# Optimization experiments

Hardware: AMD Instinct MI355X
Metric: run time of the kernel (lower is better)

Reference implementation:

```python
import jax, jax.numpy as jnp
import numpy as np

ROPE_THETA = 10000.0

def _rope(t):
    # t: (B, S, H, D) -- rotate-half RoPE over last dim
    B, S, H, D = t.shape
    inv_freq = 1.0 / (ROPE_THETA ** (jnp.arange(0, D, 2, dtype=jnp.float32) / D))  # (D/2,)
    ang = jnp.arange(S, dtype=jnp.float32)[:, None] * inv_freq[None, :]            # (S, D/2)
    cos = jnp.concatenate([jnp.cos(ang), jnp.cos(ang)], axis=-1)[None, :, None, :] # (1,S,1,D)
    sin = jnp.concatenate([jnp.sin(ang), jnp.sin(ang)], axis=-1)[None, :, None, :]
    t1, t2 = jnp.split(t, 2, axis=-1)
    rot = jnp.concatenate([-t2, t1], axis=-1)
    return t * cos.astype(t.dtype) + rot * sin.astype(t.dtype)

def setup_inputs() -> dict:
    key = jax.random.key(0)
    kx, kq, kk, kv, ko = jax.random.split(key, 5)
    B, S, DIM = 2, 2048, 2048
    x = jax.random.normal(kx, (B, S, DIM), dtype=jnp.float32)
    mask = jnp.tril(jnp.ones((S, S), dtype=bool))[None, None, :, :]  # causal (1,1,S,S)
    scale = DIM ** -0.5
    wq = jax.random.normal(kq, (DIM, DIM), dtype=jnp.float32) * scale
    wk = jax.random.normal(kk, (DIM, DIM), dtype=jnp.float32) * scale
    wv = jax.random.normal(kv, (DIM, DIM), dtype=jnp.float32) * scale
    wo = jax.random.normal(ko, (DIM, DIM), dtype=jnp.float32) * scale
    return {"x": x, "mask": mask, "wq": wq, "wk": wk, "wv": wv, "wo": wo}

def reference(x, mask, wq, wk, wv, wo):
    B, S, DIM = x.shape
    H = 16
    D = DIM // H
    scale = D ** -0.5
    # nn.Linear: y = x @ W.T
    q = (x @ wq.T).reshape(B, S, H, D)
    k = (x @ wk.T).reshape(B, S, H, D)
    v = (x @ wv.T).reshape(B, S, H, D)
    q = _rope(q)
    k = _rope(k)
    scores = jnp.einsum('bqhd,bkhd->bhqk', q, k) * scale
    scores = jnp.where(mask, scores, -jnp.inf)
    attn = jax.nn.softmax(scores, axis=-1)
    out = jnp.einsum('bhqk,bkhd->bqhd', attn, v).reshape(B, S, DIM)
    return out @ wo.T
```

## Files before the change

### kernel.cpp

```cpp
#include <hip/hip_runtime.h>
#include <cstdint>

typedef unsigned short u16;
typedef uint32_t u32;
typedef __attribute__((ext_vector_type(8))) short bf16x8;
typedef __attribute__((ext_vector_type(4))) float f32x4;
typedef __attribute__((ext_vector_type(16))) float f32x16;

#define DIM_ 2048
#define S_   2048
#define B_   2
#define H_   16
#define HD_  128
#define M_   (B_ * S_)

__device__ __forceinline__ u16 f2b(float f) {
  union { float f; uint32_t u; } v; v.f = f;
  uint32_t u = v.u;
  return (u16)((u + 0x7FFFu + ((u >> 16) & 1u)) >> 16);
}
__device__ __forceinline__ float b2f(u16 h) {
  union { uint32_t u; float f; } v; v.u = ((uint32_t)h) << 16;
  return v.f;
}

__device__ __forceinline__ u32 cvtpk(float lo, float hi) {
  u32 r;
  asm("v_cvt_pk_bf16_f32 %0, %1, %2" : "=v"(r) : "v"(lo), "v"(hi));
  return r;
}

typedef __attribute__((address_space(3))) u16 lds_u16_t;
typedef __attribute__((address_space(1))) const u16 glob_u16_t;

__device__ __forceinline__ void gload16(const u16* g, u16* l) {
  __builtin_amdgcn_global_load_lds((glob_u16_t*)g, (lds_u16_t*)l, 16, 0, 0);
}
#define GLD0(SRC, DST) \
  __builtin_amdgcn_global_load_lds((glob_u16_t*)(SRC), (lds_u16_t*)(DST), 16, 0, 0)

__global__ void convert5_kernel(const float* __restrict__ x, const float* __restrict__ wq,
                                const float* __restrict__ wk, const float* __restrict__ wv,
                                const float* __restrict__ wo, u16* __restrict__ xb,
                                u16* __restrict__ wqb, u16* __restrict__ wkb,
                                u16* __restrict__ wvb, u16* __restrict__ wob) {
  const float* src;
  u16* dst;
  int n;
  switch (blockIdx.y) {
    case 0: src = x;  dst = xb;  n = M_ * DIM_;   break;
    case 1: src = wq; dst = wqb; n = DIM_ * DIM_; break;
    case 2: src = wk; dst = wkb; n = DIM_ * DIM_; break;
    case 3: src = wv; dst = wvb; n = DIM_ * DIM_; break;
    default: src = wo; dst = wob; n = DIM_ * DIM_; break;
  }
  int i = (blockIdx.x * blockDim.x + threadIdx.x) * 4;
  const int stride = gridDim.x * blockDim.x * 4;
  for (; i < n; i += stride) {
    float4 v = *reinterpret_cast<const float4*>(src + i);
    uint64_t p = (uint64_t)f2b(v.x) | ((uint64_t)f2b(v.y) << 16) |
                 ((uint64_t)f2b(v.z) << 32) | ((uint64_t)f2b(v.w) << 48);
    *reinterpret_cast<uint64_t*>(dst + i) = p;
  }
}

__global__ void rope_table_kernel(float* __restrict__ cosT, float* __restrict__ sinT) {
  int i = blockIdx.x * blockDim.x + threadIdx.x;
  if (i >= 64 * S_) return;
  int d = i >> 11;
  int s = i & (S_ - 1);
  float inv = powf(10000.0f, -(float)d * (1.0f / 64.0f));
  float ang = (float)s * inv;
  cosT[i] = cosf(ang);
  sinT[i] = sinf(ang);
}

#define NT_ 32

#define LDA(DST, BASE)                                                         \
  _Pragma("unroll") for (int mi = 0; mi < 8; ++mi)                             \
      DST[mi] = *(const bf16x8*)((BASE) + mi * 1024);
#define LDB(DST, BASE)                                                         \
  _Pragma("unroll") for (int ni = 0; ni < NF_; ++ni)                           \
      DST[ni] = *(const bf16x8*)((BASE) +                                      \
          (BPERM_ ? (((ni) & 1) * 1024 + ((ni) >> 1) * 4096) : (ni) * 1024));

#define MFMA_KS(AV, BV)                                                        \
  _Pragma("unroll") for (int mi = 0; mi < 8; ++mi)                             \
    _Pragma("unroll") for (int ni = 0; ni < NF_; ++ni)                         \
        acc[mi][ni] = __builtin_amdgcn_mfma_f32_16x16x32_bf16(                 \
            AV[mi], BV[ni], acc[mi][ni], 0, 0, 0);

#define STAGE(BUF, OFFU) do {                                                  \
    _Pragma("unroll") for (int s = 0; s < ASW_; ++s)                           \
      GLD0(sA + goff + (OFFU) + s * (64 * DIM_),                               \
           lds + (BUF) * BUFSZ_ + s * 4096 + w * 512);                         \
    _Pragma("unroll") for (int s = 0; s < BSW_; ++s)                           \
      GLD0(sB + goff + (OFFU) + s * (64 * DIM_),                               \
           lds + (BUF) * BUFSZ_ + 16384 + s * 4096 + w * 512);                 \
  } while (0)

#define VMC_N() do {                                                           \
    if (ASW_ + BSW_ == 8) asm volatile("s_waitcnt vmcnt(8)" ::: "memory");     \
    else                  asm volatile("s_waitcnt vmcnt(6)" ::: "memory");     \
  } while (0)

#define TILE_N(BUF, NBUF, OFFU) do {                                           \
    LDA(a1, pAk1[BUF]); LDB(b1, pBk1[BUF]);                            \
    __builtin_amdgcn_sched_barrier(0);                                         \
    __builtin_amdgcn_s_setprio(1);                                             \
    MFMA_KS(a0, b0);                                                  \
    __builtin_amdgcn_s_setprio(0);                                             \
    asm volatile("s_waitcnt lgkmcnt(0)" ::: "memory");                         \
    __builtin_amdgcn_sched_barrier(0);                                         \
    __builtin_amdgcn_s_barrier();                                      \
    STAGE(BUF, OFFU);                                                          \
    __builtin_amdgcn_sched_barrier(0);                                         \
    VMC_N();                                                                   \
    __builtin_amdgcn_sched_barrier(0);                                         \
    __builtin_amdgcn_s_barrier();                                      \
    LDA(a0, pAk0[NBUF]); LDB(b0, pBk0[NBUF]);                          \
    __builtin_amdgcn_sched_barrier(0);                                         \
    __builtin_amdgcn_s_setprio(1);                                             \
    MFMA_KS(a1, b1);                                                  \
    __builtin_amdgcn_s_setprio(0);                                             \
  } while (0)

#define TILE_P(BUF, NBUF) do {                                   \
    LDA(a1, pAk1[BUF]); LDB(b1, pBk1[BUF]);                                    \
    __builtin_amdgcn_sched_barrier(0);                                         \
    __builtin_amdgcn_s_setprio(1);                                             \
    MFMA_KS(a0, b0);                                                           \
    __builtin_amdgcn_s_setprio(0);                                             \
    asm volatile("s_waitcnt lgkmcnt(0)" ::: "memory");                         \
    __builtin_amdgcn_sched_barrier(0);                                         \
    asm volatile("s_waitcnt vmcnt(0)" ::: "memory");                           \
    __builtin_amdgcn_sched_barrier(0);                                         \
    __builtin_amdgcn_s_barrier();                                              \
    LDA(a0, pAk0[NBUF]); LDB(b0, pBk0[NBUF]);                                  \
    __builtin_amdgcn_sched_barrier(0);                                         \
    __builtin_amdgcn_s_setprio(1);                                             \
    MFMA_KS(a1, b1);                                                           \
    __builtin_amdgcn_s_setprio(0);                                             \
  } while (0)

#define TILE_L(BUF) do {                                         \
    LDA(a1, pAk1[BUF]); LDB(b1, pBk1[BUF]);                                    \
    __builtin_amdgcn_sched_barrier(0);                                         \
    MFMA_KS(a0, b0);                                                           \
    MFMA_KS(a1, b1);                                                           \
  } while (0)

#define GEMM_V2_BODY(BN_, BPERM__)                                             \
  constexpr int NF_ = (BN_) / 64;                                              \
  constexpr int BPERM_ = (BPERM__);                                            \
  constexpr int ASW_ = 4;                                                      \
  constexpr int BSW_ = (BN_) / 64;                                             \
  constexpr int BUFSZ_ = 16384 + (BN_) * 64;                                   \
  const int tid = threadIdx.x;                                                 \
  const int lane = tid & 63;                                                   \
  const int w = tid >> 6;                                                      \
  const int wm = w >> 2, wn = w & 3;                                           \
  const int l15 = lane & 15, lg = lane >> 4;                                   \
  const int goff = (w * 8 + (lane >> 3)) * DIM_ + ((lane & 7) ^ (lane >> 3)) * 8; \
  const int x7 = l15 & 7;                                                      \
  const int lr0 = l15 * 64 + ((lg ^ x7) * 8);                                  \
  const int lr1 = l15 * 64 + (((4 | lg) ^ x7) * 8);                            \
  const int bbase = BPERM_ ? ((wn >> 1) * 8192 + (wn & 1) * 2048)              \
                           : (wn * ((BN_) * 16));                              \
  const u16* pAk0[2] = {lds + wm * 8192 + lr0, lds + BUFSZ_ + wm * 8192 + lr0};\
  const u16* pAk1[2] = {lds + wm * 8192 + lr1, lds + BUFSZ_ + wm * 8192 + lr1};\
  const u16* pBk0[2] = {lds + 16384 + bbase + lr0,                             \
                        lds + BUFSZ_ + 16384 + bbase + lr0};                   \
  const u16* pBk1[2] = {lds + 16384 + bbase + lr1,                             \
                        lds + BUFSZ_ + 16384 + bbase + lr1};                   \
  f32x4 acc[8][NF_];                                                           \
  _Pragma("unroll") for (int i = 0; i < 8; ++i)                                \
    _Pragma("unroll") for (int j = 0; j < NF_; ++j)                            \
        acc[i][j] = (f32x4){0.f, 0.f, 0.f, 0.f};                               \
  bf16x8 a0[8], a1[8], b0[NF_], b1[NF_];                                       \
  STAGE(0, 0);                                                                 \
  STAGE(1, 64);                                                                \
  __builtin_amdgcn_sched_barrier(0);                                           \
  VMC_N();                                                                     \
  __builtin_amdgcn_sched_barrier(0);                                           \
  __builtin_amdgcn_s_barrier();                                                \
  LDA(a0, pAk0[0]); LDB(b0, pBk0[0]);                                          \
  for (int t = 0; t < NT_ - 2; t += 2) {                                       \
    TILE_N(0, 1, 128);                                                         \
    TILE_N(1, 0, 192);                                                         \
    sA += 128; sB += 128;                                                      \
  }                                                                            \
  TILE_P(0, 1);                                                                \
  TILE_L(1);

__global__ __launch_bounds__(512, 2) void gemm256_qkv_kernel(
    const u16* __restrict__ xb, const u16* __restrict__ wqb, const u16* __restrict__ wkb,
    const u16* __restrict__ wvb, u16* __restrict__ qb, u16* __restrict__ kb,
    u16* __restrict__ vb, const float* __restrict__ cosT, const float* __restrict__ sinT) {
  __shared__ __align__(16) u16 lds[65536];

  const int bid = blockIdx.x;
  const int logical = (bid & 7) * 48 + (bid >> 3);
  const int mt = logical / 24;
  const int rem = logical % 24;
  const int z = rem >> 3;
  const int nt = rem & 7;
  const u16* Wm = (z == 0) ? wqb : (z == 1) ? wkb : wvb;
  u16* out = (z == 0) ? qb : (z == 1) ? kb : vb;

  const u16* sA = xb + (size_t)(mt * 256) * DIM_;
  const u16* sB = Wm + (size_t)(nt * 256) * DIM_;

  GEMM_V2_BODY(256, 1)

  const int colbase = nt * 256 + (wn >> 1) * 128 + (wn & 1) * 32;
  if (z < 2) {
#pragma unroll
    for (int mi = 0; mi < 8; ++mi) {
      const int row = mt * 256 + wm * 128 + mi * 16 + lg * 4;
      const int s = row & (S_ - 1);
#pragma unroll
      for (int ni = 0; ni < 2; ++ni) {
        const int d = (wn & 1) * 32 + ni * 16 + l15;
        const float4 c4 = *(const float4*)(cosT + d * S_ + s);
        const float4 s4 = *(const float4*)(sinT + d * S_ + s);
        const float cc[4]  = {c4.x, c4.y, c4.z, c4.w};
        const float ssn[4] = {s4.x, s4.y, s4.z, s4.w};
        u16* p = out + (size_t)row * DIM_ + colbase + ni * 16 + l15;
#pragma unroll
        for (int r = 0; r < 4; ++r) {
          const float t1 = acc[mi][ni][r];
          const float t2 = acc[mi][ni + 2][r];
          p[(size_t)r * DIM_]      = f2b(t1 * cc[r] - t2 * ssn[r]);
          p[(size_t)r * DIM_ + 64] = f2b(t2 * cc[r] + t1 * ssn[r]);
        }
      }
    }
  } else {
#pragma unroll
    for (int mi = 0; mi < 8; ++mi)
#pragma unroll
      for (int ni = 0; ni < 4; ++ni) {
        const int row = mt * 256 + wm * 128 + mi * 16 + lg * 4;
        const int col = colbase + (ni & 1) * 16 + (ni >> 1) * 64 + l15;
#pragma unroll
        for (int r = 0; r < 4; ++r)
          out[(size_t)(row + r) * DIM_ + col] = f2b(acc[mi][ni][r]);
      }
  }
}

__global__ __launch_bounds__(512, 2) void gemm_out_v2_kernel(const u16* __restrict__ A,
                                                             const u16* __restrict__ W,
                                                             float* __restrict__ Cf) {
  __shared__ __align__(16) u16 lds[49152];
  const int bid = blockIdx.x;
  const int logical = (bid & 7) * 32 + (bid >> 3);
  const int mt = logical >> 4;
  const int nt = logical & 15;

  const u16* sA = A + (size_t)(mt * 256) * DIM_;
  const u16* sB = W + (size_t)(nt * 128) * DIM_;

  GEMM_V2_BODY(128, 0)

#pragma unroll
  for (int mi = 0; mi < 8; ++mi)
#pragma unroll
    for (int ni = 0; ni < 2; ++ni) {
      const int row = mt * 256 + wm * 128 + mi * 16 + lg * 4;
      const int col = nt * 128 + wn * 32 + ni * 16 + l15;
#pragma unroll
      for (int r = 0; r < 4; ++r)
        Cf[(size_t)(row + r) * DIM_ + col] = acc[mi][ni][r];
    }
}

#define CEXP 0.12751744f

__global__ __launch_bounds__(256, 2) void attn_kernel(const u16* __restrict__ q,
                                                      const u16* __restrict__ k,
                                                      const u16* __restrict__ v,
                                                      u16* __restrict__ ao) {
  __shared__ __align__(16) u16 smem[32768];
  u16* kTl = smem;
  u16* vTl = smem + 16384;

  const int qt   = blockIdx.z ? (int)blockIdx.x : (int)(gridDim.x - 1 - blockIdx.x);
  const int head = blockIdx.y;
  const int b    = blockIdx.z;
  const int t = threadIdx.x;
  const int lane = t & 63;
  const int w = t >> 6;
  const int l31 = lane & 31;
  const int hi = lane >> 5;
  const int kxor = (lane & 7) << 3;
  const int qrow0 = qt * 128 + w * 32;
  const size_t bS = (size_t)b * S_;

  bf16x8 qf[8];
  {
    const u16* qrow = q + (bS + qrow0 + l31) * DIM_ + head * HD_;
#pragma unroll
    for (int st = 0; st < 8; ++st)
      qf[st] = *(const bf16x8*)(qrow + st * 16 + hi * 8);
  }

  f32x16 accO[4];
#pragma unroll
  for (int db = 0; db < 4; ++db)
#pragma unroll
    for (int rr = 0; rr < 16; ++rr) accO[db][rr] = 0.f;
  float m = -1e30f, l = 0.f;

  const int tmax_w = 2 * qt + (w >> 1);
  const int ttend = 2 * qt + 1;

  bf16x8 vv[4];

  auto stageK = [&](int buf, int tt) {
#pragma unroll
    for (int p = 0; p < 4; ++p) {
      const int cid = p * 256 + w * 64 + lane;
      const int kr = cid >> 4;
      const int cg = (cid & 15) ^ (kr & 7);
      gload16(k + (bS + tt * 64 + kr) * DIM_ + head * HD_ + cg * 8,
              kTl + buf * 8192 + (p * 256 + w * 64) * 8);
    }
  };
  auto loadV = [&](int tt) {
#pragma unroll
    for (int p = 0; p < 4; ++p) {
      const int dchunk = p * 4 + w;
      vv[p] = *(const bf16x8*)(v + (bS + tt * 64 + lane) * DIM_ + head * HD_ + dchunk * 8);
    }
  };
  auto writeV = [&](int buf) {
#pragma unroll
    for (int p = 0; p < 4; ++p) {
      const int dchunk = p * 4 + w;
#pragma unroll
      for (int j = 0; j < 8; ++j) {
        const int d = dchunk * 8 + j;
        vTl[buf * 8192 + d * 64 + (lane ^ ((d & 7) << 3))] = (u16)vv[p][j];
      }
    }
  };

  stageK(0, 0);
  loadV(0);
  writeV(0);
  __syncthreads();

  for (int tt = 0; tt <= ttend; ++tt) {
    const int cur = tt & 1;
    const int alt = cur ^ 1;

    if (tt + 1 <= ttend) {
      stageK(alt, tt + 1);
      loadV(tt + 1);
    }

    if (tt <= tmax_w) {
      const u16* kB = kTl + cur * 8192;
      const u16* vB = vTl + cur * 8192;
      f32x16 sA, sB;
#pragma unroll
      for (int rr = 0; rr < 16; ++rr) { sA[rr] = 0.f; sB[rr] = 0.f; }
      __builtin_amdgcn_s_setprio(1);
#pragma unroll
      for (int st = 0; st < 8; ++st) {
        const int dc = st * 16 + hi * 8;
        bf16x8 k0 = *(const bf16x8*)(kB + l31 * 128 + (dc ^ kxor));
        bf16x8 k1 = *(const bf16x8*)(kB + (32 + l31) * 128 + (dc ^ kxor));
        sA = __builtin_amdgcn_mfma_f32_32x32x16_bf16(k0, qf[st], sA, 0, 0, 0);
        sB = __builtin_amdgcn_mfma_f32_32x32x16_bf16(k1, qf[st], sB, 0, 0, 0);
      }
      __builtin_amdgcn_s_setprio(0);

      const int qg = qrow0 + l31;
      if (tt * 64 + 63 > qrow0) {
        const int kb = tt * 64 + 4 * hi;
#pragma unroll
        for (int rr = 0; rr < 16; ++rr) {
          const int kg = kb + (rr & 3) + 8 * (rr >> 2);
          sA[rr] = (kg <= qg) ? sA[rr] : -1e30f;
          sB[rr] = (kg + 32 <= qg) ? sB[rr] : -1e30f;
        }
      }

      float mx[8];
#pragma unroll
      for (int i = 0; i < 8; ++i)
        mx[i] = fmaxf(fmaxf(sA[i], sA[i + 8]), fmaxf(sB[i], sB[i + 8]));
#pragma unroll
      for (int i = 0; i < 4; ++i) mx[i] = fmaxf(mx[i], mx[i + 4]);
      float pm = fmaxf(fmaxf(mx[0], mx[1]), fmaxf(mx[2], mx[3]));
      pm = fmaxf(pm, __shfl_xor(pm, 32));
      const float mN = fmaxf(m, pm);
      if (!__all(pm - m <= 90.5f)) {
        const float osc = exp2f((m - mN) * CEXP);
        l *= osc;
#pragma unroll
        for (int db = 0; db < 4; ++db)
#pragma unroll
          for (int rr = 0; rr < 16; ++rr) accO[db][rr] *= osc;
        m = mN;
      }
      const float mc = m * CEXP;
      float lsv[4] = {0.f, 0.f, 0.f, 0.f};
#pragma unroll
      for (int rr = 0; rr < 16; ++rr) {
        const float pa = exp2f(__builtin_fmaf(sA[rr], CEXP, -mc));
        const float pb = exp2f(__builtin_fmaf(sB[rr], CEXP, -mc));
        sA[rr] = pa; sB[rr] = pb;
        lsv[rr & 3] += pa + pb;
      }
      float ls = (lsv[0] + lsv[1]) + (lsv[2] + lsv[3]);
      ls += __shfl_xor(ls, 32);
      l += ls;

#define PV_STEP(ARR, R0, ST2)                                                      \
      {                                                                            \
        u32 a0 = cvtpk(ARR[(R0) + 0], ARR[(R0) + 1]);                              \
        u32 a1 = cvtpk(ARR[(R0) + 2], ARR[(R0) + 3]);                              \
        u32 b0 = cvtpk(ARR[(R0) + 4], ARR[(R0) + 5]);                              \
        u32 b1 = cvtpk(ARR[(R0) + 6], ARR[(R0) + 7]);                              \
        asm("v_permlane32_swap_b32 %0, %1" : "+v"(a0), "+v"(b0));                  \
        asm("v_permlane32_swap_b32 %0, %1" : "+v"(a1), "+v"(b1));                  \
        union { u32 uu[4]; bf16x8 v8; } pf;                                        \
        pf.uu[0] = a0; pf.uu[1] = a1; pf.uu[2] = b0; pf.uu[3] = b1;                \
        const int ko = (ST2) * 16 + hi * 8;                                        \
        __builtin_amdgcn_s_setprio(1);                                             \
        _Pragma("unroll")                                                          \
        for (int db = 0; db < 4; ++db) {                                           \
          const int dr = db * 32 + l31;                                            \
          bf16x8 vf = *(const bf16x8*)(vB + dr * 64 + (ko ^ kxor));                \
          accO[db] =                                                               \
              __builtin_amdgcn_mfma_f32_32x32x16_bf16(vf, pf.v8, accO[db], 0, 0, 0); \
        }                                                                          \
        __builtin_amdgcn_s_setprio(0);                                             \
      }
      PV_STEP(sA, 0, 0)
      PV_STEP(sA, 8, 1)
      PV_STEP(sB, 0, 2)
      PV_STEP(sB, 8, 3)
#undef PV_STEP
    }

    if (tt + 1 <= ttend) writeV(alt);
    __syncthreads();
  }

  const float linv = 1.0f / l;
  u16* oT = smem + w * 4352;
#pragma unroll
  for (int db = 0; db < 4; ++db)
#pragma unroll
    for (int q4 = 0; q4 < 4; ++q4) {
      const int dbase = db * 32 + q4 * 8 + hi * 4;
      const u32 lo = cvtpk(accO[db][q4 * 4 + 0] * linv, accO[db][q4 * 4 + 1] * linv);
      const u32 hiw = cvtpk(accO[db][q4 * 4 + 2] * linv, accO[db][q4 * 4 + 3] * linv);
      *(u32*)(oT + l31 * 136 + dbase) = lo;
      *(u32*)(oT + l31 * 136 + dbase + 2) = hiw;
    }
  __syncthreads();
#pragma unroll
  for (int i = 0; i < 8; ++i) {
    const int cid = i * 64 + lane;
    const int qloc = cid >> 4;
    const int c = cid & 15;
    const bf16x8 val = *(const bf16x8*)(oT + qloc * 136 + c * 8);
    *(bf16x8*)(ao + (bS + qrow0 + qloc) * DIM_ + head * HD_ + c * 8) = val;
  }
}

extern "C" void kernel_launch(void* const* d_in, const int* in_sizes, int n_in,
                              void* d_out, int out_size, void* d_ws, size_t ws_size,
                              hipStream_t stream) {
  const float* x  = (const float*)d_in[0];
  const float* wq = (const float*)d_in[2];
  const float* wk = (const float*)d_in[3];
  const float* wv = (const float*)d_in[4];
  const float* wo = (const float*)d_in[5];

  char* ws = (char*)d_ws;
  size_t off = 0;
  auto carve = [&](size_t bytes) { char* p = ws + off; off += bytes; return p; };
  u16* xb   = (u16*)carve((size_t)M_ * DIM_ * 2);
  u16* wqb  = (u16*)carve((size_t)DIM_ * DIM_ * 2);
  u16* wkb  = (u16*)carve((size_t)DIM_ * DIM_ * 2);
  u16* wvb  = (u16*)carve((size_t)DIM_ * DIM_ * 2);
  u16* wob  = (u16*)carve((size_t)DIM_ * DIM_ * 2);
  u16* qb   = (u16*)carve((size_t)M_ * DIM_ * 2);
  u16* kb   = (u16*)carve((size_t)M_ * DIM_ * 2);
  u16* vb   = (u16*)carve((size_t)M_ * DIM_ * 2);
  u16* aob  = (u16*)carve((size_t)M_ * DIM_ * 2);
  float* cosT = (float*)carve((size_t)64 * S_ * 4);
  float* sinT = (float*)carve((size_t)64 * S_ * 4);
  if (off > ws_size) return;

  dim3 gc(1024, 5);
  convert5_kernel<<<gc, 256, 0, stream>>>(x, wq, wk, wv, wo, xb, wqb, wkb, wvb, wob);
  rope_table_kernel<<<512, 256, 0, stream>>>(cosT, sinT);

  gemm256_qkv_kernel<<<384, 512, 0, stream>>>(xb, wqb, wkb, wvb, qb, kb, vb, cosT, sinT);

  dim3 ga(16, H_, B_);
  attn_kernel<<<ga, 256, 0, stream>>>(qb, kb, vb, aob);

  gemm_out_v2_kernel<<<256, 512, 0, stream>>>(aob, wob, (float*)d_out);
}
```

Baseline: 272.6 us.

## Store V transposed from QKV GEMM and stage it asynchronously in attention

The QKV GEMM epilogue now writes V in a per-(batch, head) transposed layout [d][s], packing four bf16 values into 64-bit stores. The attention kernel then stages V^T tiles into LDS with the same direct global-to-LDS loads used for K, with XOR swizzling. This removes the register round-trip and the scalar 16-bit LDS scatter that previously transposed V inside the attention loop. In exchange, the GEMM epilogue's V stores become strided 8-byte writes spread across rows of length S, which may coalesce less well than before.

```diff
diff --git a/kernel.cpp b/kernel.cpp
--- a/kernel.cpp
+++ b/kernel.cpp
@@ -197,7 +197,7 @@
 __global__ __launch_bounds__(512, 2) void gemm256_qkv_kernel(
     const u16* __restrict__ xb, const u16* __restrict__ wqb, const u16* __restrict__ wkb,
     const u16* __restrict__ wvb, u16* __restrict__ qb, u16* __restrict__ kb,
-    u16* __restrict__ vb, const float* __restrict__ cosT, const float* __restrict__ sinT) {
+    u16* __restrict__ vtb, const float* __restrict__ cosT, const float* __restrict__ sinT) {
   __shared__ __align__(16) u16 lds[65536];
 
   const int bid = blockIdx.x;
@@ -207,7 +207,7 @@
   const int z = rem >> 3;
   const int nt = rem & 7;
   const u16* Wm = (z == 0) ? wqb : (z == 1) ? wkb : wvb;
-  u16* out = (z == 0) ? qb : (z == 1) ? kb : vb;
+  u16* out = (z == 0) ? qb : (z == 1) ? kb : vtb;
 
   const u16* sA = xb + (size_t)(mt * 256) * DIM_;
   const u16* sB = Wm + (size_t)(nt * 256) * DIM_;
@@ -239,15 +239,20 @@
     }
   } else {
 #pragma unroll
-    for (int mi = 0; mi < 8; ++mi)
+    for (int mi = 0; mi < 8; ++mi) {
+      const int grow = mt * 256 + wm * 128 + mi * 16 + lg * 4;
+      const int s0 = grow & (S_ - 1);
+      const int bq = grow >> 11;
 #pragma unroll
       for (int ni = 0; ni < 4; ++ni) {
-        const int row = mt * 256 + wm * 128 + mi * 16 + lg * 4;
         const int col = colbase + (ni & 1) * 16 + (ni >> 1) * 64 + l15;
-#pragma unroll
-        for (int r = 0; r < 4; ++r)
-          out[(size_t)(row + r) * DIM_ + col] = f2b(acc[mi][ni][r]);
-      }
+        const int h = col >> 7, d = col & 127;
+        const u32 lo  = cvtpk(acc[mi][ni][0], acc[mi][ni][1]);
+        const u32 hi2 = cvtpk(acc[mi][ni][2], acc[mi][ni][3]);
+        const uint64_t pk = (uint64_t)lo | ((uint64_t)hi2 << 32);
+        *(uint64_t*)(out + ((size_t)(bq * 16 + h) * 128 + d) * S_ + s0) = pk;
+      }
+    }
   }
 }
 
@@ -281,7 +286,7 @@
 
 __global__ __launch_bounds__(256, 2) void attn_kernel(const u16* __restrict__ q,
                                                       const u16* __restrict__ k,
-                                                      const u16* __restrict__ v,
+                                                      const u16* __restrict__ vt,
                                                       u16* __restrict__ ao) {
   __shared__ __align__(16) u16 smem[32768];
   u16* kTl = smem;
@@ -298,6 +303,7 @@
   const int kxor = (lane & 7) << 3;
   const int qrow0 = qt * 128 + w * 32;
   const size_t bS = (size_t)b * S_;
+  const size_t vhead = (size_t)(b * 16 + head) * 128 * S_;
 
   bf16x8 qf[8];
   {
@@ -316,8 +322,6 @@
 
   const int tmax_w = 2 * qt + (w >> 1);
   const int ttend = 2 * qt + 1;
-
-  bf16x8 vv[4];
 
   auto stageK = [&](int buf, int tt) {
 #pragma unroll
@@ -329,28 +333,19 @@
               kTl + buf * 8192 + (p * 256 + w * 64) * 8);
     }
   };
-  auto loadV = [&](int tt) {
+  auto stageV = [&](int buf, int tt) {
 #pragma unroll
     for (int p = 0; p < 4; ++p) {
-      const int dchunk = p * 4 + w;
-      vv[p] = *(const bf16x8*)(v + (bS + tt * 64 + lane) * DIM_ + head * HD_ + dchunk * 8);
+      const int cid = p * 256 + w * 64 + lane;
+      const int d = cid >> 3;
+      const int cg = (cid & 7) ^ (d & 7);
+      gload16(vt + vhead + (size_t)d * S_ + tt * 64 + cg * 8,
+              vTl + buf * 8192 + (p * 256 + w * 64) * 8);
     }
   };
-  auto writeV = [&](int buf) {
-#pragma unroll
-    for (int p = 0; p < 4; ++p) {
-      const int dchunk = p * 4 + w;
-#pragma unroll
-      for (int j = 0; j < 8; ++j) {
-        const int d = dchunk * 8 + j;
-        vTl[buf * 8192 + d * 64 + (lane ^ ((d & 7) << 3))] = (u16)vv[p][j];
-      }
-    }
-  };
 
   stageK(0, 0);
-  loadV(0);
-  writeV(0);
+  stageV(0, 0);
   __syncthreads();
 
   for (int tt = 0; tt <= ttend; ++tt) {
@@ -359,7 +354,7 @@
 
     if (tt + 1 <= ttend) {
       stageK(alt, tt + 1);
-      loadV(tt + 1);
+      stageV(alt, tt + 1);
     }
 
     if (tt <= tmax_w) {
@@ -449,7 +444,6 @@
 #undef PV_STEP
     }
 
-    if (tt + 1 <= ttend) writeV(alt);
     __syncthreads();
   }
 
@@ -495,7 +489,7 @@
   u16* wob  = (u16*)carve((size_t)DIM_ * DIM_ * 2);
   u16* qb   = (u16*)carve((size_t)M_ * DIM_ * 2);
   u16* kb   = (u16*)carve((size_t)M_ * DIM_ * 2);
-  u16* vb   = (u16*)carve((size_t)M_ * DIM_ * 2);
+  u16* vtb  = (u16*)carve((size_t)M_ * DIM_ * 2);
   u16* aob  = (u16*)carve((size_t)M_ * DIM_ * 2);
   float* cosT = (float*)carve((size_t)64 * S_ * 4);
   float* sinT = (float*)carve((size_t)64 * S_ * 4);
@@ -505,10 +499,10 @@
   convert5_kernel<<<gc, 256, 0, stream>>>(x, wq, wk, wv, wo, xb, wqb, wkb, wvb, wob);
   rope_table_kernel<<<512, 256, 0, stream>>>(cosT, sinT);
 
-  gemm256_qkv_kernel<<<384, 512, 0, stream>>>(xb, wqb, wkb, wvb, qb, kb, vb, cosT, sinT);
+  gemm256_qkv_kernel<<<384, 512, 0, stream>>>(xb, wqb, wkb, wvb, qb, kb, vtb, cosT, sinT);
 
   dim3 ga(16, H_, B_);
-  attn_kernel<<<ga, 256, 0, stream>>>(qb, kb, vb, aob);
+  attn_kernel<<<ga, 256, 0, stream>>>(qb, kb, vtb, aob);
 
   gemm_out_v2_kernel<<<256, 512, 0, stream>>>(aob, wob, (float*)d_out);
 }
```

Result: faster. 253.3 us (-7.1%).
